# Kernel tuning notes

Measured on AMD Instinct MI355X. Metric: run time of the kernel, lower is better.

Reference implementation:

```python
import jax, jax.numpy as jnp
import numpy as np

QLEN, MLEN, BSZ, DMODEL, NHEAD, DHEAD, DFF = 1024, 1024, 4, 1024, 16, 64, 4096
KLEN = QLEN + MLEN


def _layernorm(x, g, b, eps=1e-5):
    mu = jnp.mean(x, axis=-1, keepdims=True)
    var = jnp.var(x, axis=-1, keepdims=True)
    return (x - mu) * jax.lax.rsqrt(var + eps) * g + b


def _rel_shift(x):
    # x: [qlen, klen, bsz, nhead] -- Transformer-XL shift trick
    q, k, b, n = x.shape
    x = jnp.pad(x, ((0, 0), (1, 0), (0, 0), (0, 0)))  # [q, k+1, b, n]
    x = x.reshape(k + 1, q, b, n)[1:]
    return x.reshape(q, k, b, n)


def setup_inputs() -> dict:
    key = jax.random.key(0)
    ks = jax.random.split(key, 16)
    s = 0.02
    inp = {
        "word_embed": jax.random.normal(ks[0], (QLEN, BSZ, DMODEL), jnp.float32),
        "pos_embed": jax.random.normal(ks[1], (KLEN, DMODEL), jnp.float32),
        "bias_q": jax.random.normal(ks[2], (NHEAD, DHEAD), jnp.float32) * s,
        "bias_k": jax.random.normal(ks[3], (NHEAD, DHEAD), jnp.float32) * s,
        "memories": jax.random.normal(ks[4], (MLEN, BSZ, DMODEL), jnp.float32),
        "W_qkv": jax.random.normal(ks[5], (DMODEL, 3 * NHEAD * DHEAD), jnp.float32) * s,
        "W_r": jax.random.normal(ks[6], (DMODEL, NHEAD * DHEAD), jnp.float32) * s,
        "W_o": jax.random.normal(ks[7], (NHEAD * DHEAD, DMODEL), jnp.float32) * s,
        "ln1_g": jnp.ones((DMODEL,), jnp.float32),
        "ln1_b": jnp.zeros((DMODEL,), jnp.float32),
        "W_ff1": jax.random.normal(ks[8], (DMODEL, DFF), jnp.float32) * s,
        "b_ff1": jnp.zeros((DFF,), jnp.float32),
        "W_ff2": jax.random.normal(ks[9], (DFF, DMODEL), jnp.float32) * s,
        "b_ff2": jnp.zeros((DMODEL,), jnp.float32),
        "ln2_g": jnp.ones((DMODEL,), jnp.float32),
        "ln2_b": jnp.zeros((DMODEL,), jnp.float32),
    }
    # causal mask with memory: position i may attend to j <= i + MLEN; True = masked
    i = jnp.arange(QLEN)[:, None]
    j = jnp.arange(KLEN)[None, :]
    inp["attention_mask"] = j > (i + MLEN)
    return inp


def reference(word_embed, pos_embed, bias_q, bias_k, attention_mask, memories,
              W_qkv, W_r, W_o, ln1_g, ln1_b, W_ff1, b_ff1, W_ff2, b_ff2, ln2_g, ln2_b):
    scale = 1.0 / np.sqrt(DHEAD)
    cat = jnp.concatenate([memories, word_embed], axis=0)  # [klen, b, d]
    w_heads = cat @ W_qkv  # [klen, b, 3*n*dh]
    q, k, v = jnp.split(w_heads, 3, axis=-1)
    q = q[-QLEN:].reshape(QLEN, BSZ, NHEAD, DHEAD)
    k = k.reshape(KLEN, BSZ, NHEAD, DHEAD)
    v = v.reshape(KLEN, BSZ, NHEAD, DHEAD)
    r = (pos_embed @ W_r).reshape(KLEN, NHEAD, DHEAD)

    AC = jnp.einsum('ibnd,jbnd->ijbn', q + bias_q, k)          # content term
    BD = jnp.einsum('ibnd,jnd->ijbn', q + bias_k, r)           # position term
    BD = _rel_shift(BD)
    score = (AC + BD) * scale
    score = jnp.where(attention_mask[:, :, None, None], -1e30, score)
    prob = jax.nn.softmax(score, axis=1)
    attn_vec = jnp.einsum('ijbn,jbnd->ibnd', prob, v).reshape(QLEN, BSZ, NHEAD * DHEAD)
    attn_out = attn_vec @ W_o
    out = _layernorm(word_embed + attn_out, ln1_g, ln1_b)       # post-LN (pre_lnorm=False)

    core = jax.nn.relu(out @ W_ff1 + b_ff1) @ W_ff2 + b_ff2
    return _layernorm(out + core, ln2_g, ln2_b)
```

## Files before the change

### kernel.cpp

```cpp
#include <hip/hip_runtime.h>


typedef __bf16 bf16x8 __attribute__((ext_vector_type(8)));
typedef float f32x4 __attribute__((ext_vector_type(4)));

#define DEVI __device__ __forceinline__

DEVI unsigned short f2bf(float f) {
  union { float f; unsigned int u; } v;
  v.f = f;
  unsigned int u = v.u;
  u += 0x7fffu + ((u >> 16) & 1u);
  return (unsigned short)(u >> 16);
}

DEVI void load16(const unsigned short* g, unsigned short* l) {
  __builtin_amdgcn_global_load_lds(
      (const __attribute__((address_space(1))) unsigned int*)g,
      (__attribute__((address_space(3))) unsigned int*)l, 16, 0, 0);
}

__global__ __launch_bounds__(256) void cvt_bf16_kernel(const float* __restrict__ in,
                                                       unsigned short* __restrict__ out) {
  const int i = blockIdx.x * 256 + threadIdx.x;
  float4 v = *(const float4*)(in + (size_t)i * 4);
  ushort4 o;
  o.x = f2bf(v.x);
  o.y = f2bf(v.y);
  o.z = f2bf(v.z);
  o.w = f2bf(v.w);
  *(ushort4*)(out + (size_t)i * 4) = o;
}

template <typename T>
__global__ __launch_bounds__(256) void transpose_to_bf16(
    const T* __restrict__ in, unsigned short* __restrict__ out, int R, int C) {
  __shared__ unsigned short t[64][72];
  const int tid = threadIdx.x;
  const size_t zoff = (size_t)blockIdx.z * R * C;
  const int r0 = blockIdx.y * 64, c0 = blockIdx.x * 64;
  const T* inp = in + zoff;
  unsigned short* outp = out + zoff;
#pragma unroll
  for (int it = 0; it < 4; ++it) {
    int f = tid + 256 * it;
    int r = f >> 4;
    int c4 = (f & 15) << 2;
    if constexpr (sizeof(T) == 4) {
      float4 v = *(const float4*)((const float*)inp + (size_t)(r0 + r) * C + c0 + c4);
      t[c4 + 0][r] = f2bf(v.x);
      t[c4 + 1][r] = f2bf(v.y);
      t[c4 + 2][r] = f2bf(v.z);
      t[c4 + 3][r] = f2bf(v.w);
    } else {
      ushort4 v = *(const ushort4*)((const unsigned short*)inp + (size_t)(r0 + r) * C + c0 + c4);
      t[c4 + 0][r] = v.x;
      t[c4 + 1][r] = v.y;
      t[c4 + 2][r] = v.z;
      t[c4 + 3][r] = v.w;
    }
  }
  __syncthreads();
#pragma unroll
  for (int it = 0; it < 4; ++it) {
    int f = tid + 256 * it;
    int cc = f >> 4;
    int r4 = (f & 15) << 2;
    ushort4 o;
    o.x = t[cc][r4 + 0];
    o.y = t[cc][r4 + 1];
    o.z = t[cc][r4 + 2];
    o.w = t[cc][r4 + 3];
    *(ushort4*)(outp + (size_t)(c0 + cc) * R + r0 + r4) = o;
  }
}

struct GemmArgs {
  const unsigned short* A;
  const unsigned short* Bt;
  int row_split;
  int M, N, K;
  const float* p0;
  const float* p1;
  const float* resid;
  float* outF;
  unsigned short* o0;
  unsigned short* o1;
  unsigned short* o2;
  unsigned short* o3;
  int relu;
};

constexpr int BM = 128, BN = 128, BK = 64;

template <int EPI>
__global__ __launch_bounds__(256, 4) void gemm_kernel(GemmArgs ga) {
  __shared__ __align__(16) unsigned short As[BM * BK];
  __shared__ __align__(16) unsigned short Bs[BN * BK];

  const int n0 = blockIdx.x * BN;
  const int m0 = blockIdx.y * BM;
  if constexpr (EPI == 0) {
    if (n0 + BN <= 1024 && m0 + BM <= ga.row_split) return;
  }
  const int tid = threadIdx.x;
  const int lane = tid & 63;
  const int wv = tid >> 6;
  const int l15 = lane & 15;
  const int quad = lane >> 4;
  const int wm = wv & 1, wn = wv >> 1;
  const int K = ga.K;
  const int r8 = lane >> 3;
  const int sc = (lane & 7) ^ r8;

  const f32x4 fzero = {0.f, 0.f, 0.f, 0.f};
  f32x4 acc[4][4];
#pragma unroll
  for (int i = 0; i < 4; ++i)
#pragma unroll
    for (int j = 0; j < 4; ++j) acc[i][j] = fzero;

  const unsigned short* Ab = ga.A + (size_t)(m0 + 32 * wv + r8) * K + sc * 8;
  const unsigned short* Bb = ga.Bt + (size_t)(n0 + 32 * wv + r8) * K + sc * 8;
  const int h7 = l15 & 7;

  for (int k0 = 0; k0 < K; k0 += BK) {
    __syncthreads();
#pragma unroll
    for (int it = 0; it < 4; ++it)
      load16(Ab + (size_t)(8 * it) * K + k0, &As[(32 * wv + 8 * it) * 64]);
#pragma unroll
    for (int it = 0; it < 4; ++it)
      load16(Bb + (size_t)(8 * it) * K + k0, &Bs[(32 * wv + 8 * it) * 64]);
    __syncthreads();
#pragma unroll
    for (int ks = 0; ks < 2; ++ks) {
      bf16x8 af[4], bg[4];
#pragma unroll
      for (int mt = 0; mt < 4; ++mt)
        af[mt] = *(const bf16x8*)&As[(wm * 64 + mt * 16 + l15) * 64 +
                                     (((ks * 4 + quad) ^ h7) * 8)];
#pragma unroll
      for (int nt = 0; nt < 4; ++nt)
        bg[nt] = *(const bf16x8*)&Bs[(wn * 64 + nt * 16 + l15) * 64 +
                                     (((ks * 4 + quad) ^ h7) * 8)];
#pragma unroll
      for (int mt = 0; mt < 4; ++mt)
#pragma unroll
        for (int nt = 0; nt < 4; ++nt)
          acc[mt][nt] =
              __builtin_amdgcn_mfma_f32_16x16x32_bf16(af[mt], bg[nt], acc[mt][nt], 0, 0, 0);
    }
  }

#pragma unroll
  for (int mt = 0; mt < 4; ++mt) {
#pragma unroll
    for (int nt = 0; nt < 4; ++nt) {
#pragma unroll
      for (int r = 0; r < 4; ++r) {
        const int row = m0 + wm * 64 + mt * 16 + quad * 4 + r;
        const int col = n0 + wn * 64 + nt * 16 + l15;
        float val = acc[mt][nt][r];
        if constexpr (EPI == 0) {
          const int seq = row >> 2, b = row & 3;
          if (col < 1024) {
            if (seq >= 1024) {
              const int nh = col >> 6, d = col & 63;
              const size_t o = ((size_t)((b * 16 + nh) * 1024 + (seq - 1024))) * 64 + d;
              ga.o0[o] = f2bf(val + ga.p0[col]);
              ga.o1[o] = f2bf(val + ga.p1[col]);
            }
          } else if (col < 2048) {
            const int c = col - 1024, nh = c >> 6, d = c & 63, bn = b * 16 + nh;
            const size_t o = (size_t)bn * 131072 +
                             (size_t)(((seq >> 4) * 2 + (d >> 5)) * 512) +
                             ((((d >> 3) & 3) * 16 + (seq & 15)) * 8) + (d & 7);
            ga.o2[o] = f2bf(val);
          } else {
            const int c = col - 2048, nh = c >> 6, d = c & 63, bn = b * 16 + nh;
            const size_t o = (size_t)bn * 131072 + (size_t)((seq >> 7) * 8192) +
                             ((((seq >> 5) & 3) * 4 + (d >> 4)) * 512) +
                             ((((seq >> 3) & 3) * 16 + (d & 15)) * 8) + (seq & 7);
            ga.o3[o] = f2bf(val);
          }
        } else if constexpr (EPI == 1) {
          const int nh = col >> 6, d = col & 63, t = row;
          const size_t o = (size_t)nh * 131072 +
                           (size_t)(((t >> 4) * 2 + (d >> 5)) * 512) +
                           ((((d >> 3) & 3) * 16 + (t & 15)) * 8) + (d & 7);
          ga.o0[o] = f2bf(val);
        } else {
          if (ga.p0) val += ga.p0[col];
          if (ga.resid) val += ga.resid[(size_t)row * ga.N + col];
          if (ga.relu) val = fmaxf(val, 0.f);
          if (ga.outF) ga.outF[(size_t)row * ga.N + col] = val;
          if (ga.o0) ga.o0[(size_t)row * ga.N + col] = f2bf(val);
        }
      }
    }
  }
}

constexpr int P_LD = 136;
constexpr float CEXP = 0.18033688f;

__global__ __launch_bounds__(256, 4) void attn_kernel(
    const unsigned short* __restrict__ QQ, const unsigned short* __restrict__ QK,
    const unsigned short* __restrict__ Kf, const unsigned short* __restrict__ Vf,
    const unsigned short* __restrict__ Rf, unsigned short* __restrict__ AVb) {
  __shared__ __align__(16) unsigned short p_s[4][16 * P_LD];

  const int tid = threadIdx.x;
  const int lane = tid & 63;
  const int wv = tid >> 6;
  const int l15 = lane & 15;
  const int quad = lane >> 4;
  const int bn = blockIdx.x;
  const int iw = (blockIdx.y * 4 + wv) * 16;
  const int nh = bn & 15;
  const int bb = bn >> 4;
  unsigned short* pw = &p_s[wv][0];

  const unsigned short* kf = Kf + (size_t)bn * 131072;
  const unsigned short* vf = Vf + (size_t)bn * 131072;
  const unsigned short* rf = Rf + (size_t)nh * 131072;

  const size_t qoff = (size_t)bn * (1024 * 64) + (size_t)(iw + l15) * 64;
  const bf16x8 qq0 = *(const bf16x8*)(QQ + qoff + quad * 8);
  const bf16x8 qq1 = *(const bf16x8*)(QQ + qoff + 32 + quad * 8);
  const bf16x8 qk0 = *(const bf16x8*)(QK + qoff + quad * 8);
  const bf16x8 qk1 = *(const bf16x8*)(QK + qoff + 32 + quad * 8);

  const f32x4 fzero = {0.f, 0.f, 0.f, 0.f};
  f32x4 o_acc[4];
#pragma unroll
  for (int i = 0; i < 4; ++i) o_acc[i] = fzero;
  float lsum[4] = {0.f, 0.f, 0.f, 0.f};

  const int lane8 = lane * 8;
  const int jmax = iw + 15 + 1024;
  for (int j0 = 0; j0 <= jmax; j0 += 128) {
    const int t16b = (j0 >> 4) + 63 - (iw >> 4);
    f32x4 bd[9];
#pragma unroll
    for (int ct = 0; ct < 9; ++ct) {
      int tg = t16b + ct;
      tg = (tg < 127) ? tg : 127;
      const unsigned short* rb = rf + (size_t)(tg * 1024) + lane8;
      bf16x8 b0 = *(const bf16x8*)rb;
      bf16x8 b1 = *(const bf16x8*)(rb + 512);
      f32x4 c = fzero;
      c = __builtin_amdgcn_mfma_f32_16x16x32_bf16(qk0, b0, c, 0, 0, 0);
      c = __builtin_amdgcn_mfma_f32_16x16x32_bf16(qk1, b1, c, 0, 0, 0);
      bd[ct] = c;
    }

    const int ntb = j0 >> 4;
    f32x4 sv[8];
#pragma unroll
    for (int nt = 0; nt < 8; ++nt) {
      const unsigned short* kb = kf + (size_t)((ntb + nt) * 1024) + lane8;
      bf16x8 b0 = *(const bf16x8*)kb;
      bf16x8 b1 = *(const bf16x8*)(kb + 512);
      f32x4 c = fzero;
      c = __builtin_amdgcn_mfma_f32_16x16x32_bf16(qq0, b0, c, 0, 0, 0);
      c = __builtin_amdgcn_mfma_f32_16x16x32_bf16(qq1, b1, c, 0, 0, 0);
      sv[nt] = c;
    }

#pragma unroll
    for (int r = 0; r < 4; ++r) {
      const int il = quad * 4 + r;
      const int u = l15 + 15 - il;
      const int srcl = (lane & 48) | (u & 15);
      float w[9];
#pragma unroll
      for (int ct = 0; ct < 9; ++ct) w[ct] = __shfl(bd[ct][r], srcl, 64);
      const int ig = iw + il;
#pragma unroll
      for (int nt = 0; nt < 8; ++nt) {
        const float bdv = (u & 16) ? w[nt + 1] : w[nt];
        const int jg = j0 + nt * 16 + l15;
        float p = exp2f((sv[nt][r] + bdv) * CEXP);
        p = (jg > ig + 1024) ? 0.f : p;
        lsum[r] += p;
        pw[il * P_LD + nt * 16 + l15] = f2bf(p);
      }
    }

    const unsigned short* vb = vf + (size_t)((j0 >> 7) * 8192) + lane8;
#pragma unroll
    for (int ks = 0; ks < 4; ++ks) {
      bf16x8 ap = *(const bf16x8*)&pw[l15 * P_LD + ks * 32 + quad * 8];
#pragma unroll
      for (int nto = 0; nto < 4; ++nto) {
        bf16x8 bv = *(const bf16x8*)(vb + (ks * 4 + nto) * 512);
        o_acc[nto] = __builtin_amdgcn_mfma_f32_16x16x32_bf16(ap, bv, o_acc[nto], 0, 0, 0);
      }
    }
  }

  float linv[4];
#pragma unroll
  for (int r = 0; r < 4; ++r) {
    float l = lsum[r];
    l += __shfl_xor(l, 1, 64);
    l += __shfl_xor(l, 2, 64);
    l += __shfl_xor(l, 4, 64);
    l += __shfl_xor(l, 8, 64);
    linv[r] = 1.f / l;
  }
#pragma unroll
  for (int nto = 0; nto < 4; ++nto) {
#pragma unroll
    for (int r = 0; r < 4; ++r) {
      const int ig = iw + quad * 4 + r;
      const int d = nto * 16 + l15;
      const float val = o_acc[nto][r] * linv[r];
      AVb[(size_t)(ig * 4 + bb) * 1024 + nh * 64 + d] = f2bf(val);
    }
  }
}

__global__ __launch_bounds__(256) void ln_kernel(const float* __restrict__ x,
                                                 const float* __restrict__ g,
                                                 const float* __restrict__ bta,
                                                 float* __restrict__ outF,
                                                 unsigned short* __restrict__ outB) {
  const int row = blockIdx.x;
  const int tid = threadIdx.x;
  const float* xr = x + (size_t)row * 1024;
  const float4 v = *(const float4*)(xr + tid * 4);
  float s = v.x + v.y + v.z + v.w;
  float ss = v.x * v.x + v.y * v.y + v.z * v.z + v.w * v.w;
#pragma unroll
  for (int off = 1; off < 64; off <<= 1) {
    s += __shfl_xor(s, off, 64);
    ss += __shfl_xor(ss, off, 64);
  }
  __shared__ float red[8];
  const int wv = tid >> 6;
  if ((tid & 63) == 0) {
    red[wv] = s;
    red[4 + wv] = ss;
  }
  __syncthreads();
  s = red[0] + red[1] + red[2] + red[3];
  ss = red[4] + red[5] + red[6] + red[7];
  const float mu = s * (1.f / 1024.f);
  const float var = ss * (1.f / 1024.f) - mu * mu;
  const float rs = rsqrtf(var + 1e-5f);
  const float vv[4] = {v.x, v.y, v.z, v.w};
#pragma unroll
  for (int u = 0; u < 4; ++u) {
    const int c = tid * 4 + u;
    const float y = (vv[u] - mu) * rs * g[c] + bta[c];
    if (outF) outF[(size_t)row * 1024 + c] = y;
    if (outB) outB[(size_t)row * 1024 + c] = f2bf(y);
  }
}

extern "C" void kernel_launch(void* const* d_in, const int* in_sizes, int n_in,
                              void* d_out, int out_size, void* d_ws, size_t ws_size,
                              hipStream_t stream) {
  (void)in_sizes; (void)n_in; (void)out_size; (void)ws_size;
  const float* word_embed = (const float*)d_in[0];
  const float* pos_embed = (const float*)d_in[1];
  const float* bias_q = (const float*)d_in[2];
  const float* bias_k = (const float*)d_in[3];
  const float* memories = (const float*)d_in[4];
  const float* W_qkv = (const float*)d_in[5];
  const float* W_r = (const float*)d_in[6];
  const float* W_o = (const float*)d_in[7];
  const float* ln1_g = (const float*)d_in[8];
  const float* ln1_b = (const float*)d_in[9];
  const float* W_ff1 = (const float*)d_in[10];
  const float* b_ff1 = (const float*)d_in[11];
  const float* W_ff2 = (const float*)d_in[12];
  const float* b_ff2 = (const float*)d_in[13];
  const float* ln2_g = (const float*)d_in[14];
  const float* ln2_b = (const float*)d_in[15];
  float* out = (float*)d_out;

  char* ws = (char*)d_ws;
  unsigned short* QQ = (unsigned short*)(ws + 0);
  unsigned short* QK = (unsigned short*)(ws + 8388608);
  unsigned short* Kf = (unsigned short*)(ws + 16777216);
  unsigned short* Vf = (unsigned short*)(ws + 50331648);
  unsigned short* Rf = (unsigned short*)(ws + 67108864);
  unsigned short* AVb = (unsigned short*)(ws + 71303168);
  float* X1 = (float*)(ws + 79691776);
  float* OUT1 = (float*)(ws + 96468992);
  unsigned short* OUT1b = (unsigned short*)(ws + 113246208);
  unsigned short* Wqkv_t = (unsigned short*)(ws + 121634816);
  unsigned short* Wr_t = (unsigned short*)(ws + 127926272);
  unsigned short* Wo_t = (unsigned short*)(ws + 130023424);
  unsigned short* Wff1_t = (unsigned short*)(ws + 132120576);
  unsigned short* Wff2_t = (unsigned short*)(ws + 140509184);
  unsigned short* Catb = (unsigned short*)(ws + 79691776);
  unsigned short* Posb = (unsigned short*)(ws + 96468992);
  unsigned short* H = (unsigned short*)(ws + 0);
  float* C2 = X1;

  const dim3 blk(256);

  cvt_bf16_kernel<<<4096, blk, 0, stream>>>(memories, Catb);
  cvt_bf16_kernel<<<4096, blk, 0, stream>>>(word_embed, Catb + (size_t)4096 * 1024);
  cvt_bf16_kernel<<<2048, blk, 0, stream>>>(pos_embed, Posb);

  transpose_to_bf16<float><<<dim3(48, 16, 1), blk, 0, stream>>>(W_qkv, Wqkv_t, 1024, 3072);
  transpose_to_bf16<float><<<dim3(16, 16, 1), blk, 0, stream>>>(W_r, Wr_t, 1024, 1024);
  transpose_to_bf16<float><<<dim3(16, 16, 1), blk, 0, stream>>>(W_o, Wo_t, 1024, 1024);
  transpose_to_bf16<float><<<dim3(64, 16, 1), blk, 0, stream>>>(W_ff1, Wff1_t, 1024, 4096);
  transpose_to_bf16<float><<<dim3(16, 64, 1), blk, 0, stream>>>(W_ff2, Wff2_t, 4096, 1024);

  {
    GemmArgs a{};
    a.A = Catb;
    a.row_split = 4096;
    a.Bt = Wqkv_t;
    a.M = 8192; a.N = 3072; a.K = 1024;
    a.p0 = bias_q; a.p1 = bias_k;
    a.o0 = QQ; a.o1 = QK; a.o2 = Kf; a.o3 = Vf;
    gemm_kernel<0><<<dim3(24, 64), blk, 0, stream>>>(a);
  }
  {
    GemmArgs a{};
    a.A = Posb;
    a.Bt = Wr_t;
    a.M = 2048; a.N = 1024; a.K = 1024;
    a.o0 = Rf;
    gemm_kernel<1><<<dim3(8, 16), blk, 0, stream>>>(a);
  }

  attn_kernel<<<dim3(64, 16), blk, 0, stream>>>(QQ, QK, Kf, Vf, Rf, AVb);

  {
    GemmArgs a{};
    a.A = AVb;
    a.Bt = Wo_t;
    a.M = 4096; a.N = 1024; a.K = 1024;
    a.resid = word_embed;
    a.outF = X1;
    gemm_kernel<2><<<dim3(8, 32), blk, 0, stream>>>(a);
  }
  ln_kernel<<<4096, blk, 0, stream>>>(X1, ln1_g, ln1_b, OUT1, OUT1b);

  {
    GemmArgs a{};
    a.A = OUT1b;
    a.Bt = Wff1_t;
    a.M = 4096; a.N = 4096; a.K = 1024;
    a.p0 = b_ff1;
    a.relu = 1;
    a.o0 = H;
    gemm_kernel<2><<<dim3(32, 32), blk, 0, stream>>>(a);
  }
  {
    GemmArgs a{};
    a.A = H;
    a.Bt = Wff2_t;
    a.M = 4096; a.N = 1024; a.K = 4096;
    a.p0 = b_ff2;
    a.resid = OUT1;
    a.outF = C2;
    gemm_kernel<2><<<dim3(8, 32), blk, 0, stream>>>(a);
  }
  ln_kernel<<<4096, blk, 0, stream>>>(C2, ln2_g, ln2_b, out, nullptr);
}
```

Baseline: 684.9 us.

## Compact QKV GEMM grid, narrow N-tiles for small GEMMs, add attention setprio

The QKV projection GEMM now uses a flat 1D grid that maps only the tiles it needs, so the early-exit blocks no longer launch. The GEMM kernel gains a WN template parameter, and the three N=1024 GEMMs use 64-wide N tiles to double the block count and fill more CUs. The attention kernel wraps its MFMA sections in s_setprio so matrix work gets issue priority over other waves. Narrower tiles cost more A-tile reloads per output, and the priority hints may not help.

```diff
diff --git a/kernel.cpp b/kernel.cpp
--- a/kernel.cpp
+++ b/kernel.cpp
@@ -91,17 +91,31 @@
   int relu;
 };
 
-constexpr int BM = 128, BN = 128, BK = 64;
-
-template <int EPI>
+constexpr int BM = 128, BK = 64;
+
+template <int EPI, int WN = 4>
 __global__ __launch_bounds__(256, 4) void gemm_kernel(GemmArgs ga) {
+  constexpr int BN_ = WN * 32;
   __shared__ __align__(16) unsigned short As[BM * BK];
-  __shared__ __align__(16) unsigned short Bs[BN * BK];
-
-  const int n0 = blockIdx.x * BN;
-  const int m0 = blockIdx.y * BM;
+  __shared__ __align__(16) unsigned short Bs[BN_ * BK];
+
+  int m0, n0;
   if constexpr (EPI == 0) {
-    if (n0 + BN <= 1024 && m0 + BM <= ga.row_split) return;
+    const int flat = blockIdx.x;
+    int mt_, nt_;
+    if (flat < 1024) {
+      mt_ = flat >> 4;
+      nt_ = 8 + (flat & 15);
+    } else {
+      const int f2 = flat - 1024;
+      mt_ = 32 + (f2 >> 3);
+      nt_ = f2 & 7;
+    }
+    m0 = mt_ * 128;
+    n0 = nt_ * 128;
+  } else {
+    n0 = blockIdx.x * BN_;
+    m0 = blockIdx.y * BM;
   }
   const int tid = threadIdx.x;
   const int lane = tid & 63;
@@ -114,14 +128,14 @@
   const int sc = (lane & 7) ^ r8;
 
   const f32x4 fzero = {0.f, 0.f, 0.f, 0.f};
-  f32x4 acc[4][4];
+  f32x4 acc[4][WN];
 #pragma unroll
   for (int i = 0; i < 4; ++i)
 #pragma unroll
-    for (int j = 0; j < 4; ++j) acc[i][j] = fzero;
+    for (int j = 0; j < WN; ++j) acc[i][j] = fzero;
 
   const unsigned short* Ab = ga.A + (size_t)(m0 + 32 * wv + r8) * K + sc * 8;
-  const unsigned short* Bb = ga.Bt + (size_t)(n0 + 32 * wv + r8) * K + sc * 8;
+  const unsigned short* Bb = ga.Bt + (size_t)(n0 + (BN_ / 4) * wv + r8) * K + sc * 8;
   const int h7 = l15 & 7;
 
   for (int k0 = 0; k0 < K; k0 += BK) {
@@ -130,24 +144,24 @@
     for (int it = 0; it < 4; ++it)
       load16(Ab + (size_t)(8 * it) * K + k0, &As[(32 * wv + 8 * it) * 64]);
 #pragma unroll
-    for (int it = 0; it < 4; ++it)
-      load16(Bb + (size_t)(8 * it) * K + k0, &Bs[(32 * wv + 8 * it) * 64]);
+    for (int it = 0; it < BN_ / 32; ++it)
+      load16(Bb + (size_t)(8 * it) * K + k0, &Bs[((BN_ / 4) * wv + 8 * it) * 64]);
     __syncthreads();
 #pragma unroll
     for (int ks = 0; ks < 2; ++ks) {
-      bf16x8 af[4], bg[4];
+      bf16x8 af[4], bg[WN];
 #pragma unroll
       for (int mt = 0; mt < 4; ++mt)
         af[mt] = *(const bf16x8*)&As[(wm * 64 + mt * 16 + l15) * 64 +
                                      (((ks * 4 + quad) ^ h7) * 8)];
 #pragma unroll
-      for (int nt = 0; nt < 4; ++nt)
-        bg[nt] = *(const bf16x8*)&Bs[(wn * 64 + nt * 16 + l15) * 64 +
+      for (int nt = 0; nt < WN; ++nt)
+        bg[nt] = *(const bf16x8*)&Bs[(wn * (WN * 16) + nt * 16 + l15) * 64 +
                                      (((ks * 4 + quad) ^ h7) * 8)];
 #pragma unroll
       for (int mt = 0; mt < 4; ++mt)
 #pragma unroll
-        for (int nt = 0; nt < 4; ++nt)
+        for (int nt = 0; nt < WN; ++nt)
           acc[mt][nt] =
               __builtin_amdgcn_mfma_f32_16x16x32_bf16(af[mt], bg[nt], acc[mt][nt], 0, 0, 0);
     }
@@ -156,11 +170,11 @@
 #pragma unroll
   for (int mt = 0; mt < 4; ++mt) {
 #pragma unroll
-    for (int nt = 0; nt < 4; ++nt) {
+    for (int nt = 0; nt < WN; ++nt) {
 #pragma unroll
       for (int r = 0; r < 4; ++r) {
         const int row = m0 + wm * 64 + mt * 16 + quad * 4 + r;
-        const int col = n0 + wn * 64 + nt * 16 + l15;
+        const int col = n0 + wn * (WN * 16) + nt * 16 + l15;
         float val = acc[mt][nt][r];
         if constexpr (EPI == 0) {
           const int seq = row >> 2, b = row & 3;
@@ -242,6 +256,7 @@
   const int jmax = iw + 15 + 1024;
   for (int j0 = 0; j0 <= jmax; j0 += 128) {
     const int t16b = (j0 >> 4) + 63 - (iw >> 4);
+    __builtin_amdgcn_s_setprio(1);
     f32x4 bd[9];
 #pragma unroll
     for (int ct = 0; ct < 9; ++ct) {
@@ -268,6 +283,7 @@
       c = __builtin_amdgcn_mfma_f32_16x16x32_bf16(qq1, b1, c, 0, 0, 0);
       sv[nt] = c;
     }
+    __builtin_amdgcn_s_setprio(0);
 
 #pragma unroll
     for (int r = 0; r < 4; ++r) {
@@ -290,6 +306,7 @@
     }
 
     const unsigned short* vb = vf + (size_t)((j0 >> 7) * 8192) + lane8;
+    __builtin_amdgcn_s_setprio(1);
 #pragma unroll
     for (int ks = 0; ks < 4; ++ks) {
       bf16x8 ap = *(const bf16x8*)&pw[l15 * P_LD + ks * 32 + quad * 8];
@@ -299,6 +316,7 @@
         o_acc[nto] = __builtin_amdgcn_mfma_f32_16x16x32_bf16(ap, bv, o_acc[nto], 0, 0, 0);
       }
     }
+    __builtin_amdgcn_s_setprio(0);
   }
 
   float linv[4];
@@ -418,12 +436,11 @@
   {
     GemmArgs a{};
     a.A = Catb;
-    a.row_split = 4096;
     a.Bt = Wqkv_t;
     a.M = 8192; a.N = 3072; a.K = 1024;
     a.p0 = bias_q; a.p1 = bias_k;
     a.o0 = QQ; a.o1 = QK; a.o2 = Kf; a.o3 = Vf;
-    gemm_kernel<0><<<dim3(24, 64), blk, 0, stream>>>(a);
+    gemm_kernel<0><<<dim3(1280), blk, 0, stream>>>(a);
   }
   {
     GemmArgs a{};
@@ -431,7 +448,7 @@
     a.Bt = Wr_t;
     a.M = 2048; a.N = 1024; a.K = 1024;
     a.o0 = Rf;
-    gemm_kernel<1><<<dim3(8, 16), blk, 0, stream>>>(a);
+    gemm_kernel<1, 2><<<dim3(16, 16), blk, 0, stream>>>(a);
   }
 
   attn_kernel<<<dim3(64, 16), blk, 0, stream>>>(QQ, QK, Kf, Vf, Rf, AVb);
@@ -443,7 +460,7 @@
     a.M = 4096; a.N = 1024; a.K = 1024;
     a.resid = word_embed;
     a.outF = X1;
-    gemm_kernel<2><<<dim3(8, 32), blk, 0, stream>>>(a);
+    gemm_kernel<2, 2><<<dim3(16, 32), blk, 0, stream>>>(a);
   }
   ln_kernel<<<4096, blk, 0, stream>>>(X1, ln1_g, ln1_b, OUT1, OUT1b);
 
@@ -465,7 +482,7 @@
     a.p0 = b_ff2;
     a.resid = OUT1;
     a.outF = C2;
-    gemm_kernel<2><<<dim3(8, 32), blk, 0, stream>>>(a);
+    gemm_kernel<2, 2><<<dim3(16, 32), blk, 0, stream>>>(a);
   }
   ln_kernel<<<4096, blk, 0, stream>>>(C2, ln2_g, ln2_b, out, nullptr);
 }
```

After: 724.3 us. 1.06x slower.
